# Kernel tuning notes

Hardware: AMD Instinct MI355X
Metric: run time of the kernel (lower is better)

The kernel has to match this reference:

```python
import jax, jax.numpy as jnp
import numpy as np

EMBED_DIM = 1024
NUM_HEADS = 16
HEAD_DIM = EMBED_DIM // NUM_HEADS
BSZ, TGT, SRC = 4, 2048, 2048


def setup_inputs() -> dict:
    key = jax.random.key(0)
    ks = jax.random.split(key, 8)
    s = EMBED_DIM ** -0.5  # keep activations O(1)
    return {
        "query": jax.random.normal(ks[0], (BSZ, TGT, EMBED_DIM), jnp.float32),
        "key": jax.random.normal(ks[1], (BSZ, SRC, EMBED_DIM), jnp.float32),
        "key_padding_mask": jnp.ones((BSZ, SRC), jnp.float32),
        "Wq": jax.random.normal(ks[2], (EMBED_DIM, EMBED_DIM), jnp.float32) * s,
        "bq": jnp.zeros((EMBED_DIM,), jnp.float32),
        "Wk": jax.random.normal(ks[3], (EMBED_DIM, EMBED_DIM), jnp.float32) * s,
        "bk": jnp.zeros((EMBED_DIM,), jnp.float32),
        "Wv": jax.random.normal(ks[4], (EMBED_DIM, EMBED_DIM), jnp.float32) * s,
        "bv": jnp.zeros((EMBED_DIM,), jnp.float32),
        "Wo": jax.random.normal(ks[5], (EMBED_DIM, EMBED_DIM), jnp.float32) * s,
        "bo": jnp.zeros((EMBED_DIM,), jnp.float32),
    }


def _split_heads(x, bsz, seqlen):
    # [b, s, e] -> [b, h, s, d]
    return x.reshape(bsz, seqlen, NUM_HEADS, HEAD_DIM).transpose(0, 2, 1, 3)


def reference(query, key, key_padding_mask, Wq, bq, Wk, bk, Wv, bv, Wo, bo):
    bsz, src_len, embed_dim = key.shape
    tgt_len = query.shape[1]
    scaling = HEAD_DIM ** -0.5

    q = (query @ Wq.T + bq) * scaling                # [b, t, e]
    k = key @ Wk.T + bk                              # [b, s, e]
    v = key @ Wv.T + bv                              # [b, s, e]

    qh = _split_heads(q, bsz, tgt_len)               # [b, h, t, d]
    kh = _split_heads(k, bsz, src_len)               # [b, h, s, d]
    vh = _split_heads(v, bsz, src_len)               # [b, h, s, d]

    scores = jnp.einsum('bhtd,bhsd->bhts', qh, kh)   # [b, h, t, s]

    # _expand_mask: additive mask, 0 where mask==1, finfo.min where mask==0
    inv = 1.0 - key_padding_mask.astype(scores.dtype)
    neg = jnp.finfo(scores.dtype).min
    add_mask = jnp.where(inv.astype(bool), neg, inv)  # [b, s]
    scores = scores + add_mask[:, None, None, :]

    probs = jax.nn.softmax(scores, axis=-1)          # dropout p=0 / eval -> identity

    out = jnp.einsum('bhts,bhsd->bhtd', probs, vh)   # [b, h, t, d]
    out = out.transpose(0, 2, 1, 3).reshape(bsz, tgt_len, embed_dim)
    return out @ Wo.T + bo
```

## Files before the change

### kernel.cpp

```cpp
#include <hip/hip_runtime.h>

typedef unsigned short u16;
typedef __attribute__((ext_vector_type(8))) short bf16x8;
typedef __attribute__((ext_vector_type(4))) float f32x4;
typedef __attribute__((ext_vector_type(16))) float f32x16;

#define LOG2E 1.44269504088896f

__device__ inline u16 f2b(float f) {
  union { float f; unsigned u; } x; x.f = f;
  unsigned r = x.u + 0x7fffu + ((x.u >> 16) & 1u);
  return (u16)(r >> 16);
}

__device__ inline void gload_lds16(const void* g, void* l) {
  __builtin_amdgcn_global_load_lds(
      (__attribute__((address_space(1))) void*)(g),
      (__attribute__((address_space(3))) void*)(l), 16, 0, 0);
}

__device__ inline unsigned cvtpk_bf16(float lo, float hi_) {
  unsigned r;
  asm("v_cvt_pk_bf16_f32 %0, %1, %2" : "=v"(r) : "v"(lo), "v"(hi_));
  return r;
}
__device__ inline float exp2_hw(float x) { return __builtin_amdgcn_exp2f(x); }

__global__ __launch_bounds__(256) void cvt_all(
    const float* __restrict__ q, const float* __restrict__ k,
    const float* __restrict__ wq, const float* __restrict__ wk,
    const float* __restrict__ wv, const float* __restrict__ wo,
    u16* __restrict__ qb, u16* __restrict__ kb,
    u16* __restrict__ wqb, u16* __restrict__ wkb,
    u16* __restrict__ wvb, u16* __restrict__ wob) {
  int b = blockIdx.x;
  const float* in;
  u16* out;
  if (b < 8192) {
    in = q; out = qb;
  } else if (b < 16384) {
    in = k; out = kb; b -= 8192;
  } else {
    const int w = (b - 16384) >> 10;
    b = (b - 16384) & 1023;
    in = (w == 0) ? wq : (w == 1) ? wk : (w == 2) ? wv : wo;
    out = (w == 0) ? wqb : (w == 1) ? wkb : (w == 2) ? wvb : wob;
  }
  const int i = b * 256 + threadIdx.x;
  const float4 v = ((const float4*)in)[i];
  union { u16 s[4]; uint2 u; } o;
  o.s[0] = f2b(v.x); o.s[1] = f2b(v.y); o.s[2] = f2b(v.z); o.s[3] = f2b(v.w);
  ((uint2*)out)[i] = o.u;
}


__global__ __launch_bounds__(256) void gemm_o(
    const u16* __restrict__ A, const u16* __restrict__ W,
    const float* __restrict__ bias, float* __restrict__ Cout,
    int K) {
  __shared__ __align__(16) u16 lA[2][128 * 64];
  __shared__ __align__(16) u16 lW[2][128 * 64];
  const int tid = threadIdx.x, lane = tid & 63, wid = tid >> 6;
  const int wr = wid >> 1, wc = wid & 1;
  const int fr = lane & 15, fq = lane >> 4;
  const size_t abase = (size_t)blockIdx.x * 128 * K;
  const size_t wbase = (size_t)blockIdx.y * 128 * K;

  f32x4 acc[4][4];
#pragma unroll
  for (int i = 0; i < 4; ++i)
#pragma unroll
    for (int j = 0; j < 4; ++j) acc[i][j] = (f32x4){0.f, 0.f, 0.f, 0.f};

#define GSTAGE(bufi, kt)                                                          \
  do {                                                                            \
    _Pragma("unroll")                                                             \
    for (int is = 0; is < 4; ++is) {                                              \
      const int c = is * 256 + tid;                                               \
      const int r = c >> 3, ch = (c & 7) ^ (r & 7);                               \
      gload_lds16(A + abase + (size_t)r * K + (kt) + ch * 8, lA[bufi] + c * 8);   \
      gload_lds16(W + wbase + (size_t)r * K + (kt) + ch * 8, lW[bufi] + c * 8);   \
    }                                                                             \
  } while (0)

  GSTAGE(0, 0);
  __syncthreads();

  int buf = 0;
  for (int kt = 0; kt < K; kt += 64) {
    if (kt + 64 < K) GSTAGE(buf ^ 1, kt + 64);
#pragma unroll
    for (int kk = 0; kk < 2; ++kk) {
      bf16x8 af[4], wf[4];
#pragma unroll
      for (int m = 0; m < 4; ++m) {
        const int row = wr * 64 + m * 16 + fr;
        af[m] = *(const bf16x8*)&lA[buf][row * 64 + (((kk * 4 + fq) ^ (row & 7)) << 3)];
      }
#pragma unroll
      for (int n = 0; n < 4; ++n) {
        const int row = wc * 64 + n * 16 + fr;
        wf[n] = *(const bf16x8*)&lW[buf][row * 64 + (((kk * 4 + fq) ^ (row & 7)) << 3)];
      }
#pragma unroll
      for (int m = 0; m < 4; ++m)
#pragma unroll
        for (int n = 0; n < 4; ++n)
          acc[m][n] = __builtin_amdgcn_mfma_f32_16x16x32_bf16(af[m], wf[n], acc[m][n], 0, 0, 0);
    }
    __syncthreads();
    buf ^= 1;
  }
#undef GSTAGE

  const int row0 = blockIdx.x * 128 + wr * 64 + fq * 4;
  const int col0 = blockIdx.y * 128 + wc * 64 + fr;
#pragma unroll
  for (int n = 0; n < 4; ++n) {
    const int col = col0 + n * 16;
    const float bb = bias[col];
#pragma unroll
    for (int m = 0; m < 4; ++m) {
#pragma unroll
      for (int r = 0; r < 4; ++r) {
        const int row = row0 + m * 16 + r;
        Cout[(size_t)row * 1024 + col] = acc[m][n][r] + bb;
      }
    }
  }
}

__global__ __launch_bounds__(256) void gemm_qkv(
    const u16* __restrict__ qA, const u16* __restrict__ kA,
    const u16* __restrict__ Wq, const u16* __restrict__ Wk,
    const u16* __restrict__ Wv, const float* __restrict__ bq,
    const float* __restrict__ bk, const float* __restrict__ bv,
    u16* __restrict__ Qout, u16* __restrict__ Kout,
    u16* __restrict__ Vtout, int K) {
  __shared__ __align__(16) u16 lA[2][128 * 64];
  __shared__ __align__(16) u16 lW[2][128 * 64];
  const int tid = threadIdx.x, lane = tid & 63, wid = tid >> 6;
  const int wr = wid >> 1, wc = wid & 1;
  const int fr = lane & 15, fq = lane >> 4;
  const int path = blockIdx.y >> 3, ny = blockIdx.y & 7;
  const u16* A = (path == 0) ? qA : kA;
  const u16* W = (path == 0) ? Wq : (path == 1) ? Wk : Wv;
  const float* bias = (path == 0) ? bq : (path == 1) ? bk : bv;
  const size_t abase = (size_t)blockIdx.x * 128 * K;
  const size_t wbase = (size_t)ny * 128 * K;

  f32x4 acc[4][4];
#pragma unroll
  for (int i = 0; i < 4; ++i)
#pragma unroll
    for (int j = 0; j < 4; ++j) acc[i][j] = (f32x4){0.f, 0.f, 0.f, 0.f};

#define GSTAGE(bufi, kt)                                                          \
  do {                                                                            \
    _Pragma("unroll")                                                             \
    for (int is = 0; is < 4; ++is) {                                              \
      const int c = is * 256 + tid;                                               \
      const int r = c >> 3, ch = (c & 7) ^ (r & 7);                               \
      gload_lds16(A + abase + (size_t)r * K + (kt) + ch * 8, lA[bufi] + c * 8);   \
      gload_lds16(W + wbase + (size_t)r * K + (kt) + ch * 8, lW[bufi] + c * 8);   \
    }                                                                             \
  } while (0)

  GSTAGE(0, 0);
  __syncthreads();

  int buf = 0;
  for (int kt = 0; kt < K; kt += 64) {
    if (kt + 64 < K) GSTAGE(buf ^ 1, kt + 64);
#pragma unroll
    for (int kk = 0; kk < 2; ++kk) {
      bf16x8 af[4], wf[4];
#pragma unroll
      for (int m = 0; m < 4; ++m) {
        const int row = wr * 64 + m * 16 + fr;
        af[m] = *(const bf16x8*)&lA[buf][row * 64 + (((kk * 4 + fq) ^ (row & 7)) << 3)];
      }
#pragma unroll
      for (int n = 0; n < 4; ++n) {
        const int row = wc * 64 + n * 16 + fr;
        wf[n] = *(const bf16x8*)&lW[buf][row * 64 + (((kk * 4 + fq) ^ (row & 7)) << 3)];
      }
#pragma unroll
      for (int m = 0; m < 4; ++m)
#pragma unroll
        for (int n = 0; n < 4; ++n)
          acc[m][n] = __builtin_amdgcn_mfma_f32_16x16x32_bf16(af[m], wf[n], acc[m][n], 0, 0, 0);
    }
    __syncthreads();
    buf ^= 1;
  }
#undef GSTAGE

  if (path == 2) {
    const int bI = blockIdx.x >> 4;
    const int srow0 = ((blockIdx.x * 128) & 2047) + wr * 64 + fq * 4;
    const int col0 = ny * 128 + wc * 64 + fr;
#pragma unroll
    for (int n = 0; n < 4; ++n) {
      const int col = col0 + n * 16;
      const float bb = bias[col];
      const int h = col >> 6, dl = col & 63;
      u16* vrow = Vtout + ((size_t)((bI * 16 + h) * 64 + dl)) * 2048;
#pragma unroll
      for (int m = 0; m < 4; ++m) {
        const int s = srow0 + m * 16;
        const int x = s & 15;
        const int pos = (((s & 63) >> 4) * 2 + ((x >> 2) & 1)) * 8 + ((x & 3) | ((x & 8) >> 1));
        union { u16 s4[4]; uint2 u; } w;
#pragma unroll
        for (int r = 0; r < 4; ++r) w.s4[r] = f2b(acc[m][n][r] + bb);
        *(uint2*)&vrow[(s >> 6) * 64 + pos] = w.u;
      }
    }
  } else {
    const float alpha = (path == 0) ? 0.125f * LOG2E : 1.0f;
    u16* Cout = (path == 0) ? Qout : Kout;
    const int row0 = blockIdx.x * 128 + wr * 64 + fq * 4;
    const int col0 = ny * 128 + wc * 64 + fr;
#pragma unroll
    for (int n = 0; n < 4; ++n) {
      const int col = col0 + n * 16;
      const float bb = bias[col];
#pragma unroll
      for (int m = 0; m < 4; ++m) {
#pragma unroll
        for (int r = 0; r < 4; ++r) {
          const int row = row0 + m * 16 + r;
          Cout[(size_t)row * 1024 + col] = f2b((acc[m][n][r] + bb) * alpha);
        }
      }
    }
  }
}

__global__ __launch_bounds__(512, 4) void flash16(
    const u16* __restrict__ Qb, const u16* __restrict__ Kb,
    const u16* __restrict__ Vt, const float* __restrict__ mask,
    u16* __restrict__ Ob) {
  __shared__ __align__(16) u16 Kl[2][4096];
  __shared__ __align__(16) u16 Vl[2][4096];
  __shared__ unsigned long long bml[32];
  __shared__ float lbuf[8][32];

  const int f = blockIdx.x;
  const int xcd = f & 7, i = f >> 3;
  const int bh = xcd * 8 + (i >> 3);
  const int qt = i & 7;
  const int b = bh >> 4, h = bh & 15;
  const int tid = threadIdx.x, lane = tid & 63, wid = tid >> 6;
  const int l31 = lane & 31, hi = lane >> 5;
  const int qrow0 = qt * 256 + wid * 32;

  bf16x8 qf[4];
  {
    const u16* qp = Qb + ((size_t)(b * 2048 + qrow0 + l31)) * 1024 + h * 64;
#pragma unroll
    for (int dc = 0; dc < 4; ++dc) qf[dc] = *(const bf16x8*)(qp + dc * 16 + hi * 8);
  }

  const u16* kbase = Kb + ((size_t)(b * 2048)) * 1024 + h * 64;
  const u16* vbase = Vt + ((size_t)(bh * 64)) * 2048;
  const float* mrow = mask + b * 2048;

  const int l31s = tid & 31, his = (tid >> 5) & 1, mid = (tid >> 6) & 3,
            top = (tid >> 8) & 1;
  const int koff = (top * 32 + l31s) * 1024 + (mid * 2 + his) * 8;
  const int voff = (top * 32 + l31s) * 2048 + (mid * 2 + his) * 8;

  f32x16 o0 = {}, o1 = {};
  float l_r = 0.f;

#define STAGE(bufi, tt)                               \
  do {                                                \
    const u16* kb_t = kbase + (size_t)(tt) * 65536;   \
    const u16* vb_t = vbase + (tt) * 64;              \
    gload_lds16(kb_t + koff, &Kl[bufi][tid * 8]);     \
    gload_lds16(vb_t + voff, &Vl[bufi][tid * 8]);     \
  } while (0)

  STAGE(0, 0);

#pragma unroll
  for (int tt = 0; tt < 4; ++tt) {
    const int tile = wid * 4 + tt;
    const unsigned long long bmv = __ballot(mrow[tile * 64 + lane] == 1.0f);
    if (lane == 0) bml[tile] = bmv;
  }
  __syncthreads();

  const unsigned mflags =
      (unsigned)__ballot(lane < 32 && bml[lane] != ~0ull);

  for (int t = 0; t < 32; ++t) {
    const int cur = t & 1;
    if (t + 1 < 32) STAGE(cur ^ 1, t + 1);

    const u16* Kc = Kl[cur];
    const u16* Vc = Vl[cur];

#pragma unroll
    for (int n = 0; n < 2; ++n) {
      f32x16 acc = {};
#pragma unroll
      for (int dc = 0; dc < 4; ++dc) {
        const bf16x8 kf = *(const bf16x8*)&Kc[(n * 4 + dc) * 512 + lane * 8];
        acc = __builtin_amdgcn_mfma_f32_32x32x16_bf16(kf, qf[dc], acc, 0, 0, 0);
      }

#pragma unroll
      for (int reg = 0; reg < 16; ++reg) acc[reg] = exp2_hw(acc[reg]);

      if (mflags & (1u << t)) {
        const unsigned long long bm = bml[t];
#pragma unroll
        for (int reg = 0; reg < 16; ++reg) {
          const int k = n * 32 + (reg & 3) + 8 * (reg >> 2) + 4 * hi;
          if (!((bm >> k) & 1)) acc[reg] = 0.f;
        }
      }

      {
        float s0a = (acc[0] + acc[1]) + (acc[2] + acc[3]);
        float s1a = (acc[4] + acc[5]) + (acc[6] + acc[7]);
        float s2a = (acc[8] + acc[9]) + (acc[10] + acc[11]);
        float s3a = (acc[12] + acc[13]) + (acc[14] + acc[15]);
        l_r += (s0a + s1a) + (s2a + s3a);
      }

      bf16x8 pa0, pa1;
      {
        union { unsigned u[4]; bf16x8 v; } pk;
#pragma unroll
        for (int j = 0; j < 4; ++j) pk.u[j] = cvtpk_bf16(acc[2 * j], acc[2 * j + 1]);
        pa0 = pk.v;
#pragma unroll
        for (int j = 0; j < 4; ++j) pk.u[j] = cvtpk_bf16(acc[8 + 2 * j], acc[9 + 2 * j]);
        pa1 = pk.v;
      }

      {
        const bf16x8 v00 = *(const bf16x8*)&Vc[(0 * 4 + n * 2 + 0) * 512 + lane * 8];
        const bf16x8 v01 = *(const bf16x8*)&Vc[(0 * 4 + n * 2 + 1) * 512 + lane * 8];
        o0 = __builtin_amdgcn_mfma_f32_32x32x16_bf16(pa0, v00, o0, 0, 0, 0);
        o0 = __builtin_amdgcn_mfma_f32_32x32x16_bf16(pa1, v01, o0, 0, 0, 0);
      }
      {
        const bf16x8 v10 = *(const bf16x8*)&Vc[(1 * 4 + n * 2 + 0) * 512 + lane * 8];
        const bf16x8 v11 = *(const bf16x8*)&Vc[(1 * 4 + n * 2 + 1) * 512 + lane * 8];
        o1 = __builtin_amdgcn_mfma_f32_32x32x16_bf16(pa0, v10, o1, 0, 0, 0);
        o1 = __builtin_amdgcn_mfma_f32_32x32x16_bf16(pa1, v11, o1, 0, 0, 0);
      }
    }

    __syncthreads();
  }
#undef STAGE

  const float l_tot = l_r + __shfl_xor(l_r, 32);
  const float linv = 1.0f / l_tot;
  if (!hi) lbuf[wid][l31] = linv;
  __builtin_amdgcn_wave_barrier();
  float lv[16];
#pragma unroll
  for (int reg = 0; reg < 16; ++reg)
    lv[reg] = lbuf[wid][(reg & 3) + 8 * (reg >> 2) + 4 * hi];

  u16* ob = Ob + ((size_t)(b * 2048 + qrow0)) * 1024 + h * 64 + l31;
#pragma unroll
  for (int reg = 0; reg < 16; ++reg) {
    const int q = (reg & 3) + 8 * (reg >> 2) + 4 * hi;
    ob[(size_t)q * 1024] = f2b(o0[reg] * lv[reg]);
    ob[(size_t)q * 1024 + 32] = f2b(o1[reg] * lv[reg]);
  }
}

extern "C" void kernel_launch(void* const* d_in, const int* in_sizes, int n_in,
                              void* d_out, int out_size, void* d_ws, size_t ws_size,
                              hipStream_t stream) {
  const float* query = (const float*)d_in[0];
  const float* keyin = (const float*)d_in[1];
  const float* maskp = (const float*)d_in[2];
  const float* Wq = (const float*)d_in[3];
  const float* bq = (const float*)d_in[4];
  const float* Wk = (const float*)d_in[5];
  const float* bk = (const float*)d_in[6];
  const float* Wv = (const float*)d_in[7];
  const float* bv = (const float*)d_in[8];
  const float* Wo = (const float*)d_in[9];
  const float* bo = (const float*)d_in[10];

  char* ws = (char*)d_ws;
  const size_t ACT = (size_t)8192 * 1024 * 2;
  const size_t WMAT = (size_t)1024 * 1024 * 2;
  u16* qbf = (u16*)(ws);
  u16* kbf = (u16*)(ws + ACT);
  u16* wqb = (u16*)(ws + 2 * ACT);
  u16* wkb = (u16*)(ws + 2 * ACT + WMAT);
  u16* wvb = (u16*)(ws + 2 * ACT + 2 * WMAT);
  u16* wob = (u16*)(ws + 2 * ACT + 3 * WMAT);
  u16* Qb  = (u16*)(ws + 2 * ACT + 4 * WMAT);
  u16* Kb  = (u16*)(ws + 3 * ACT + 4 * WMAT);
  u16* VtDed = (u16*)(ws + 4 * ACT + 4 * WMAT);
  u16* attnb = kbf;

  cvt_all<<<20480, 256, 0, stream>>>(query, keyin, Wq, Wk, Wv, Wo,
                                     qbf, kbf, wqb, wkb, wvb, wob);

  gemm_qkv<<<dim3(64, 24), 256, 0, stream>>>(qbf, kbf, wqb, wkb, wvb,
                                             bq, bk, bv, Qb, Kb, VtDed, 1024);

  flash16<<<512, 512, 0, stream>>>(Qb, Kb, VtDed, maskp, attnb);

  gemm_o<<<dim3(64, 8), 256, 0, stream>>>(attnb, wob, bo, (float*)d_out, 1024);
}
```

Before: 183.6 us.

## Fuse activation fp32-to-bf16 conversion into QKV GEMM A-tile loading

```diff
diff --git a/kernel.cpp b/kernel.cpp
--- a/kernel.cpp
+++ b/kernel.cpp
@@ -26,33 +26,22 @@
 }
 __device__ inline float exp2_hw(float x) { return __builtin_amdgcn_exp2f(x); }
 
-__global__ __launch_bounds__(256) void cvt_all(
-    const float* __restrict__ q, const float* __restrict__ k,
+__global__ __launch_bounds__(256) void cvt_w(
     const float* __restrict__ wq, const float* __restrict__ wk,
     const float* __restrict__ wv, const float* __restrict__ wo,
-    u16* __restrict__ qb, u16* __restrict__ kb,
     u16* __restrict__ wqb, u16* __restrict__ wkb,
     u16* __restrict__ wvb, u16* __restrict__ wob) {
   int b = blockIdx.x;
-  const float* in;
-  u16* out;
-  if (b < 8192) {
-    in = q; out = qb;
-  } else if (b < 16384) {
-    in = k; out = kb; b -= 8192;
-  } else {
-    const int w = (b - 16384) >> 10;
-    b = (b - 16384) & 1023;
-    in = (w == 0) ? wq : (w == 1) ? wk : (w == 2) ? wv : wo;
-    out = (w == 0) ? wqb : (w == 1) ? wkb : (w == 2) ? wvb : wob;
-  }
+  const int w = b >> 10;
+  b &= 1023;
+  const float* in = (w == 0) ? wq : (w == 1) ? wk : (w == 2) ? wv : wo;
+  u16* out = (w == 0) ? wqb : (w == 1) ? wkb : (w == 2) ? wvb : wob;
   const int i = b * 256 + threadIdx.x;
   const float4 v = ((const float4*)in)[i];
   union { u16 s[4]; uint2 u; } o;
   o.s[0] = f2b(v.x); o.s[1] = f2b(v.y); o.s[2] = f2b(v.z); o.s[3] = f2b(v.w);
   ((uint2*)out)[i] = o.u;
 }
-
 
 __global__ __launch_bounds__(256) void gemm_o(
     const u16* __restrict__ A, const u16* __restrict__ W,
@@ -131,7 +120,7 @@
 }
 
 __global__ __launch_bounds__(256) void gemm_qkv(
-    const u16* __restrict__ qA, const u16* __restrict__ kA,
+    const float* __restrict__ qA32, const float* __restrict__ kA32,
     const u16* __restrict__ Wq, const u16* __restrict__ Wk,
     const u16* __restrict__ Wv, const float* __restrict__ bq,
     const float* __restrict__ bk, const float* __restrict__ bv,
@@ -143,7 +132,7 @@
   const int wr = wid >> 1, wc = wid & 1;
   const int fr = lane & 15, fq = lane >> 4;
   const int path = blockIdx.y >> 3, ny = blockIdx.y & 7;
-  const u16* A = (path == 0) ? qA : kA;
+  const float* A32 = (path == 0) ? qA32 : kA32;
   const u16* W = (path == 0) ? Wq : (path == 1) ? Wk : Wv;
   const float* bias = (path == 0) ? bq : (path == 1) ? bk : bv;
   const size_t abase = (size_t)blockIdx.x * 128 * K;
@@ -155,23 +144,56 @@
 #pragma unroll
     for (int j = 0; j < 4; ++j) acc[i][j] = (f32x4){0.f, 0.f, 0.f, 0.f};
 
-#define GSTAGE(bufi, kt)                                                          \
-  do {                                                                            \
-    _Pragma("unroll")                                                             \
-    for (int is = 0; is < 4; ++is) {                                              \
-      const int c = is * 256 + tid;                                               \
-      const int r = c >> 3, ch = (c & 7) ^ (r & 7);                               \
-      gload_lds16(A + abase + (size_t)r * K + (kt) + ch * 8, lA[bufi] + c * 8);   \
-      gload_lds16(W + wbase + (size_t)r * K + (kt) + ch * 8, lW[bufi] + c * 8);   \
-    }                                                                             \
+  float4 areg[8];
+
+#define ALOAD(kt)                                                                  \
+  do {                                                                             \
+    _Pragma("unroll")                                                              \
+    for (int is = 0; is < 4; ++is) {                                               \
+      const int p = is * 256 + tid;                                                \
+      const int r = p >> 3, gch = p & 7;                                           \
+      const float* src = A32 + abase + (size_t)r * K + (kt) + gch * 8;             \
+      areg[2 * is] = ((const float4*)src)[0];                                      \
+      areg[2 * is + 1] = ((const float4*)src)[1];                                  \
+    }                                                                              \
   } while (0)
 
-  GSTAGE(0, 0);
+#define AWRITE(bufi)                                                               \
+  do {                                                                             \
+    _Pragma("unroll")                                                              \
+    for (int is = 0; is < 4; ++is) {                                               \
+      const int p = is * 256 + tid;                                                \
+      const int r = p >> 3, gch = p & 7;                                           \
+      union { unsigned u[4]; uint4 v; } pk;                                        \
+      pk.u[0] = cvtpk_bf16(areg[2 * is].x, areg[2 * is].y);                        \
+      pk.u[1] = cvtpk_bf16(areg[2 * is].z, areg[2 * is].w);                        \
+      pk.u[2] = cvtpk_bf16(areg[2 * is + 1].x, areg[2 * is + 1].y);                \
+      pk.u[3] = cvtpk_bf16(areg[2 * is + 1].z, areg[2 * is + 1].w);                \
+      *(uint4*)&lA[bufi][(r * 8 + (gch ^ (r & 7))) * 8] = pk.v;                    \
+    }                                                                              \
+  } while (0)
+
+#define WSTAGE(bufi, kt)                                                           \
+  do {                                                                             \
+    _Pragma("unroll")                                                              \
+    for (int is = 0; is < 4; ++is) {                                               \
+      const int c = is * 256 + tid;                                                \
+      const int r = c >> 3, ch = (c & 7) ^ (r & 7);                                \
+      gload_lds16(W + wbase + (size_t)r * K + (kt) + ch * 8, lW[bufi] + c * 8);    \
+    }                                                                              \
+  } while (0)
+
+  ALOAD(0);
+  WSTAGE(0, 0);
+  AWRITE(0);
   __syncthreads();
 
   int buf = 0;
   for (int kt = 0; kt < K; kt += 64) {
-    if (kt + 64 < K) GSTAGE(buf ^ 1, kt + 64);
+    if (kt + 64 < K) {
+      ALOAD(kt + 64);
+      WSTAGE(buf ^ 1, kt + 64);
+    }
 #pragma unroll
     for (int kk = 0; kk < 2; ++kk) {
       bf16x8 af[4], wf[4];
@@ -191,10 +213,13 @@
         for (int n = 0; n < 4; ++n)
           acc[m][n] = __builtin_amdgcn_mfma_f32_16x16x32_bf16(af[m], wf[n], acc[m][n], 0, 0, 0);
     }
+    if (kt + 64 < K) AWRITE(buf ^ 1);
     __syncthreads();
     buf ^= 1;
   }
-#undef GSTAGE
+#undef ALOAD
+#undef AWRITE
+#undef WSTAGE
 
   if (path == 2) {
     const int bI = blockIdx.x >> 4;
@@ -397,8 +422,6 @@
   char* ws = (char*)d_ws;
   const size_t ACT = (size_t)8192 * 1024 * 2;
   const size_t WMAT = (size_t)1024 * 1024 * 2;
-  u16* qbf = (u16*)(ws);
-  u16* kbf = (u16*)(ws + ACT);
   u16* wqb = (u16*)(ws + 2 * ACT);
   u16* wkb = (u16*)(ws + 2 * ACT + WMAT);
   u16* wvb = (u16*)(ws + 2 * ACT + 2 * WMAT);
@@ -406,12 +429,11 @@
   u16* Qb  = (u16*)(ws + 2 * ACT + 4 * WMAT);
   u16* Kb  = (u16*)(ws + 3 * ACT + 4 * WMAT);
   u16* VtDed = (u16*)(ws + 4 * ACT + 4 * WMAT);
-  u16* attnb = kbf;
-
-  cvt_all<<<20480, 256, 0, stream>>>(query, keyin, Wq, Wk, Wv, Wo,
-                                     qbf, kbf, wqb, wkb, wvb, wob);
-
-  gemm_qkv<<<dim3(64, 24), 256, 0, stream>>>(qbf, kbf, wqb, wkb, wvb,
+  u16* attnb = (u16*)(ws + ACT);
+
+  cvt_w<<<4096, 256, 0, stream>>>(Wq, Wk, Wv, Wo, wqb, wkb, wvb, wob);
+
+  gemm_qkv<<<dim3(64, 24), 256, 0, stream>>>(query, keyin, wqb, wkb, wvb,
                                              bq, bk, bv, Qb, Kb, VtDed, 1024);
 
   flash16<<<512, 512, 0, stream>>>(Qb, Kb, VtDed, maskp, attnb);
```

New measurement: 189.0 us. +3.0%, slower.
